# Kernel tuning notes

Hardware: AMD Instinct MI355X
Metric: run time of the kernel (lower is better)

Reference implementation:

```python
import jax, jax.numpy as jnp
import numpy as np

NUM_BINS = 22
TEMPLATE_DIM = 16
MAX_DIST = 40.0
LN_EPS = 1e-5


def setup_inputs() -> dict:
    key = jax.random.key(0)
    k1, k2, k3, k4, k5, k6 = jax.random.split(key, 6)
    B, N = 2, 1024
    template_coords = jax.random.normal(k1, (B, N, 3), dtype=jnp.float32) * 10.0  # Angstrom-ish scale
    confidence = jax.random.uniform(k2, (B, N), dtype=jnp.float32)
    # projection = Linear(22 -> 16) + LayerNorm(16)
    lim = 1.0 / np.sqrt(NUM_BINS)
    W = jax.random.uniform(k3, (NUM_BINS, TEMPLATE_DIM), minval=-lim, maxval=lim, dtype=jnp.float32)
    b = jax.random.uniform(k4, (TEMPLATE_DIM,), minval=-lim, maxval=lim, dtype=jnp.float32)
    gamma = jnp.ones((TEMPLATE_DIM,), dtype=jnp.float32)
    beta = jnp.zeros((TEMPLATE_DIM,), dtype=jnp.float32)
    return {"template_coords": template_coords, "confidence": confidence,
            "W": W, "b": b, "gamma": gamma, "beta": beta}


def reference(template_coords, confidence, W, b, gamma, beta):
    num_dist_bins = NUM_BINS - 1          # 21
    bin_width = MAX_DIST / num_dist_bins
    bin_edges = jnp.arange(0.0, MAX_DIST, bin_width, dtype=jnp.float32)  # (21,)
    no_template_bin = NUM_BINS - 1

    # pairwise distances (B, N, N)
    diff = template_coords[:, :, None, :] - template_coords[:, None, :, :]
    dist = jnp.sqrt(jnp.sum(diff * diff, axis=-1) + 1e-8)

    # torch.bucketize(right=False) == searchsorted side='left'
    binned = jnp.searchsorted(bin_edges, dist, side="left")
    binned = jnp.clip(binned, 0, NUM_BINS - 2)

    has_i = (confidence > 0)[:, :, None]
    has_j = (confidence > 0)[:, None, :]
    binned = jnp.where(has_i & has_j, binned, no_template_bin)

    one_hot = jax.nn.one_hot(binned, NUM_BINS, dtype=jnp.float32)  # (B,N,N,22)

    # Linear + LayerNorm + ReLU
    h = jnp.einsum("bijk,kd->bijd", one_hot, W) + b
    mu = jnp.mean(h, axis=-1, keepdims=True)
    var = jnp.mean((h - mu) ** 2, axis=-1, keepdims=True)
    h = (h - mu) * jax.lax.rsqrt(var + LN_EPS) * gamma + beta
    h = jax.nn.relu(h)

    conf_pair = jnp.minimum(confidence[:, :, None], confidence[:, None, :])
    return h * conf_pair[..., None]
```

## Files before the change

### kernel.cpp

```cpp
#include <hip/hip_runtime.h>

#define BATCH 2
#define N 1024
#define NBINS 22
#define TDIM 16
#define TSTR 20

__global__ __launch_bounds__(256) void te_enc(
    const float* __restrict__ coords,
    const float* __restrict__ confp,
    const float* __restrict__ Wp,
    const float* __restrict__ bp,
    const float* __restrict__ gp,
    const float* __restrict__ betap,
    float* __restrict__ out)
{
    __shared__ __align__(16) float tbl[NBINS * TSTR];

    const int tid = threadIdx.x;
    const int blk = blockIdx.x;
    const int batch = blk >> 10;
    const int i = blk & (N - 1);

    if (tid < NBINS) {
        float h[TDIM];
        float sum = 0.f;
        #pragma unroll
        for (int d = 0; d < TDIM; ++d) {
            h[d] = Wp[tid * TDIM + d] + bp[d];
            sum += h[d];
        }
        const float mu = sum * (1.f / TDIM);
        float s2 = 0.f;
        #pragma unroll
        for (int d = 0; d < TDIM; ++d) {
            const float t = h[d] - mu;
            s2 += t * t;
        }
        const float rs = 1.f / sqrtf(s2 * (1.f / TDIM) + 1e-5f);
        #pragma unroll
        for (int d = 0; d < TDIM; ++d) {
            const float v = (h[d] - mu) * rs * gp[d] + betap[d];
            tbl[tid * TSTR + d] = fmaxf(v, 0.f);
        }
    }
    __syncthreads();

    const float xi = coords[(batch * N + i) * 3 + 0];
    const float yi = coords[(batch * N + i) * 3 + 1];
    const float zi = coords[(batch * N + i) * 3 + 2];
    const float ci = confp[batch * N + i];

    float* orow = out + (((size_t)batch * N + i) * N) * TDIM;
    const float* jc = coords + batch * N * 3;
    const float* jf = confp + batch * N;

    #pragma unroll
    for (int it = 0; it < 4; ++it) {
        const int j = tid + it * 256;
        const float xj = jc[j * 3 + 0];
        const float yj = jc[j * 3 + 1];
        const float zj = jc[j * 3 + 2];
        const float cj = jf[j];

        const float dx = __fsub_rn(xi, xj);
        const float dy = __fsub_rn(yi, yj);
        const float dz = __fsub_rn(zi, zj);
        float s = __fmul_rn(dx, dx);
        s = __fadd_rn(s, __fmul_rn(dy, dy));
        s = __fadd_rn(s, __fmul_rn(dz, dz));
        s = __fadd_rn(s, 1e-8f);
        const float dist = __fsqrt_rn(s);

        int idx = 1;
        #pragma unroll
        for (int k = 1; k <= 20; ++k) {
            const float ek = (float)k * (float)(40.0 / 21.0);
            idx += (ek < dist) ? 1 : 0;
        }
        int bin = idx < 20 ? idx : 20;
        if (!(ci > 0.f && cj > 0.f)) bin = NBINS - 1;
        const float cm = fminf(ci, cj);

        const float4* row = (const float4*)&tbl[bin * TSTR];
        const float4 r0 = row[0], r1 = row[1], r2 = row[2], r3 = row[3];

        float4 o0, o1, o2, o3;
        o0.x = r0.x * cm; o0.y = r0.y * cm; o0.z = r0.z * cm; o0.w = r0.w * cm;
        o1.x = r1.x * cm; o1.y = r1.y * cm; o1.z = r1.z * cm; o1.w = r1.w * cm;
        o2.x = r2.x * cm; o2.y = r2.y * cm; o2.z = r2.z * cm; o2.w = r2.w * cm;
        o3.x = r3.x * cm; o3.y = r3.y * cm; o3.z = r3.z * cm; o3.w = r3.w * cm;

        float4* dst = (float4*)(orow + (size_t)j * TDIM);
        dst[0] = o0;
        dst[1] = o1;
        dst[2] = o2;
        dst[3] = o3;
    }
}

extern "C" void kernel_launch(void* const* d_in, const int* in_sizes, int n_in,
                              void* d_out, int out_size, void* d_ws, size_t ws_size,
                              hipStream_t stream) {
    const float* coords = (const float*)d_in[0];
    const float* conf   = (const float*)d_in[1];
    const float* W      = (const float*)d_in[2];
    const float* b      = (const float*)d_in[3];
    const float* g      = (const float*)d_in[4];
    const float* beta   = (const float*)d_in[5];
    float* out          = (float*)d_out;

    te_enc<<<dim3(BATCH * N), dim3(256), 0, stream>>>(coords, conf, W, b, g, beta, out);
}
```

Measured before the change: 160.4 us.

## Stage j-coordinates in LDS and coalesce output stores across lanes

Each block now loads all j coordinates and confidences of its batch into shared memory once. The store pattern is remapped so that four lanes cooperate on one j, each writing one float4 of the 16-dim output. Consecutive lanes therefore write contiguous 16-byte chunks and a wave store is fully coalesced, replacing the strided 64-byte-per-lane writes. The cost is four times more distance and bin computations per output, since each lane recomputes for its j, plus extra LDS traffic.

```diff
diff --git a/kernel.cpp b/kernel.cpp
--- a/kernel.cpp
+++ b/kernel.cpp
@@ -16,11 +16,24 @@
     float* __restrict__ out)
 {
     __shared__ __align__(16) float tbl[NBINS * TSTR];
+    __shared__ float lx[N], ly[N], lz[N], lc[N];
 
     const int tid = threadIdx.x;
     const int blk = blockIdx.x;
     const int batch = blk >> 10;
     const int i = blk & (N - 1);
+
+    const float* jc = coords + batch * N * 3;
+    const float* jf = confp + batch * N;
+
+    #pragma unroll
+    for (int q = 0; q < 4; ++q) {
+        const int j = tid + q * 256;
+        lx[j] = jc[j * 3 + 0];
+        ly[j] = jc[j * 3 + 1];
+        lz[j] = jc[j * 3 + 2];
+        lc[j] = jf[j];
+    }
 
     if (tid < NBINS) {
         float h[TDIM];
@@ -51,51 +64,49 @@
     const float zi = coords[(batch * N + i) * 3 + 2];
     const float ci = confp[batch * N + i];
 
-    float* orow = out + (((size_t)batch * N + i) * N) * TDIM;
-    const float* jc = coords + batch * N * 3;
-    const float* jf = confp + batch * N;
+    const int w  = tid >> 6;
+    const int l  = tid & 63;
+    const int lq = l >> 2;
+    const int sub = l & 3;
+
+    float4* orow4 = (float4*)out + ((size_t)(batch * N + i)) * (N * TDIM / 4);
 
     #pragma unroll
     for (int it = 0; it < 4; ++it) {
-        const int j = tid + it * 256;
-        const float xj = jc[j * 3 + 0];
-        const float yj = jc[j * 3 + 1];
-        const float zj = jc[j * 3 + 2];
-        const float cj = jf[j];
+        const int j_base = it * 256 + w * 64;
+        #pragma unroll
+        for (int c = 0; c < 4; ++c) {
+            const int j = j_base + 16 * c + lq;
+            const float xj = lx[j];
+            const float yj = ly[j];
+            const float zj = lz[j];
+            const float cj = lc[j];
 
-        const float dx = __fsub_rn(xi, xj);
-        const float dy = __fsub_rn(yi, yj);
-        const float dz = __fsub_rn(zi, zj);
-        float s = __fmul_rn(dx, dx);
-        s = __fadd_rn(s, __fmul_rn(dy, dy));
-        s = __fadd_rn(s, __fmul_rn(dz, dz));
-        s = __fadd_rn(s, 1e-8f);
-        const float dist = __fsqrt_rn(s);
+            const float dx = __fsub_rn(xi, xj);
+            const float dy = __fsub_rn(yi, yj);
+            const float dz = __fsub_rn(zi, zj);
+            float s = __fmul_rn(dx, dx);
+            s = __fadd_rn(s, __fmul_rn(dy, dy));
+            s = __fadd_rn(s, __fmul_rn(dz, dz));
+            s = __fadd_rn(s, 1e-8f);
+            const float dist = __fsqrt_rn(s);
 
-        int idx = 1;
-        #pragma unroll
-        for (int k = 1; k <= 20; ++k) {
-            const float ek = (float)k * (float)(40.0 / 21.0);
-            idx += (ek < dist) ? 1 : 0;
+            int idx = 1;
+            #pragma unroll
+            for (int k = 1; k <= 20; ++k) {
+                const float ek = (float)k * (float)(40.0 / 21.0);
+                idx += (ek < dist) ? 1 : 0;
+            }
+            int bin = idx < 20 ? idx : 20;
+            if (!(ci > 0.f && cj > 0.f)) bin = NBINS - 1;
+            const float cm = fminf(ci, cj);
+
+            const float4 r = *(const float4*)&tbl[bin * TSTR + sub * 4];
+            float4 o;
+            o.x = r.x * cm; o.y = r.y * cm; o.z = r.z * cm; o.w = r.w * cm;
+
+            orow4[j_base * 4 + 64 * c + l] = o;
         }
-        int bin = idx < 20 ? idx : 20;
-        if (!(ci > 0.f && cj > 0.f)) bin = NBINS - 1;
-        const float cm = fminf(ci, cj);
-
-        const float4* row = (const float4*)&tbl[bin * TSTR];
-        const float4 r0 = row[0], r1 = row[1], r2 = row[2], r3 = row[3];
-
-        float4 o0, o1, o2, o3;
-        o0.x = r0.x * cm; o0.y = r0.y * cm; o0.z = r0.z * cm; o0.w = r0.w * cm;
-        o1.x = r1.x * cm; o1.y = r1.y * cm; o1.z = r1.z * cm; o1.w = r1.w * cm;
-        o2.x = r2.x * cm; o2.y = r2.y * cm; o2.z = r2.z * cm; o2.w = r2.w * cm;
-        o3.x = r3.x * cm; o3.y = r3.y * cm; o3.z = r3.z * cm; o3.w = r3.w * cm;
-
-        float4* dst = (float4*)(orow + (size_t)j * TDIM);
-        dst[0] = o0;
-        dst[1] = o1;
-        dst[2] = o2;
-        dst[3] = o3;
     }
 }
 
```

Result: faster. 147.7 us (-7.9%).
